# Optimization experiments

Hardware: AMD Instinct MI355X
Metric: run time of the kernel (lower is better)

Reference implementation:

```python
import jax, jax.numpy as jnp
import numpy as np

N_VERTICES = 24  # hardcoded via torch.eye(24) in the original
K = 3


def normalized_adj(adj):
    # scipy version: L = (A @ D^-1/2).T @ D^-1/2 = D^-1/2 @ A^T @ D^-1/2
    d = adj.sum(axis=1)
    d_inv_sqrt = jnp.where(d > 0, 1.0 / jnp.sqrt(d), 0.0)
    return (adj * d_inv_sqrt[None, :]).T * d_inv_sqrt[None, :]


def cheb_polynomials(L, k_order):
    Ts = [jnp.eye(N_VERTICES, dtype=L.dtype), L]
    for _ in range(2, k_order):
        Ts.append(2.0 * L @ Ts[-1] - Ts[-2])
    return jnp.stack(Ts[:k_order])  # (K, N, N)


def setup_inputs() -> dict:
    key = jax.random.key(0)
    k1, k2, k3 = jax.random.split(key, 3)
    x = jax.random.normal(k1, (64, 32, N_VERTICES, 512), dtype=jnp.float32)
    adj = jax.random.uniform(k2, (N_VERTICES, N_VERTICES), dtype=jnp.float32)
    Theta = jax.random.normal(k3, (K, 32, 32), dtype=jnp.float32)
    return {"x": x, "adj": adj, "Theta": Theta}


def reference(x, adj, Theta):
    # x: (b, c, n, t); adj: (n, n); Theta: (K, c, o)
    L = normalized_adj(adj)
    T = cheb_polynomials(L, K)  # (K, n, m)
    # original per-timestep, per-k: rhs[b,m,c] = sum_n x[b,n,c] T_k[n,m];
    # out[b,m,o] += rhs @ Theta_k. Fused over t and k, final permute -> (b,o,m,t).
    out = jnp.einsum('knm,bcnt,kco->bomt', T, x, Theta)
    return out
```

## Files before the change

### kernel.cpp

```cpp
#include <hip/hip_runtime.h>
#include <hip/hip_bf16.h>
#include <stdint.h>


#define NV 24
#define CIN 32
#define COUT 32
#define TDIM 512
#define BATCH 64
#define MDIM 768
#define KD 768
#define BK 32
#define NKT (KD / BK)
#define BM 128
#define BLOB (BM * BK)
#define BT 64
#define KUN (KD / 8)
#define FSTR 66

typedef __attribute__((ext_vector_type(8))) short short8v;
typedef __attribute__((ext_vector_type(4))) float float4v;

__device__ inline unsigned short f2bf(float f) {
    unsigned int u = __float_as_uint(f);
    unsigned int r = (u + 0x7fffu + ((u >> 16) & 1u)) >> 16;
    return (unsigned short)r;
}

__global__ __launch_bounds__(256) void prep_w(const float* __restrict__ adj,
                                              const float* __restrict__ Theta,
                                              unsigned short* __restrict__ Wp) {
    __shared__ float adjS[NV * NV];
    __shared__ float disS[NV];
    __shared__ float LS[NV * NV];
    __shared__ float T2S[NV * NV];
    int tid = threadIdx.x;
    for (int e = tid; e < NV * NV; e += 256) adjS[e] = adj[e];
    __syncthreads();
    if (tid < NV) {
        float d = 0.f;
        for (int j = 0; j < NV; ++j) d += adjS[tid * NV + j];
        disS[tid] = (d > 0.f) ? rsqrtf(d) : 0.f;
    }
    __syncthreads();
    for (int e = tid; e < NV * NV; e += 256) {
        int i = e / NV, j = e % NV;
        LS[e] = disS[i] * adjS[j * NV + i] * disS[j];
    }
    __syncthreads();
    for (int e = tid; e < NV * NV; e += 256) {
        int i = e / NV, j = e % NV;
        float s = 0.f;
        for (int p = 0; p < NV; ++p) s += LS[i * NV + p] * LS[p * NV + j];
        T2S[e] = 2.f * s - (i == j ? 1.f : 0.f);
    }
    __syncthreads();
    int r0 = blockIdx.x * (MDIM / 64);
    for (int e = tid; e < (MDIM / 64) * KD; e += 256) {
        int lr = e / KD, col = e % KD;
        int row = r0 + lr;
        int o = row / NV, m = row % NV;
        int c = col / NV, n = col % NV;
        float th0 = Theta[0 * CIN * COUT + c * COUT + o];
        float th1 = Theta[1 * CIN * COUT + c * COUT + o];
        float th2 = Theta[2 * CIN * COUT + c * COUT + o];
        float v = (n == m ? th0 : 0.f) + LS[n * NV + m] * th1 + T2S[n * NV + m] * th2;
        size_t idx = (((size_t)(row >> 7) * NKT + (col >> 5)) * BM + (row & 127)) * BK + (col & 31);
        Wp[idx] = f2bf(v);
    }
}

#define GSTEP(KT, AC, AN)                                                      \
    do {                                                                       \
        int kx = (((KT) * 4 + quad) ^ s7);                                     \
        short8v bb[4];                                                         \
        _Pragma("unroll")                                                      \
        for (int j = 0; j < 4; ++j) bb[j] = Bsv[tj[j] + kx];                   \
        if ((KT) + 1 < NKT) {                                                  \
            _Pragma("unroll")                                                  \
            for (int i = 0; i < 6; ++i) AN[i] = Apv[aoff[i] + ((KT) + 1) * 512]; \
        }                                                                      \
        _Pragma("unroll")                                                      \
        for (int i = 0; i < 6; ++i)                                            \
            _Pragma("unroll")                                                  \
            for (int j = 0; j < 4; ++j)                                        \
                acc[i][j] = __builtin_amdgcn_mfma_f32_16x16x32_bf16(           \
                    AC[i], bb[j], acc[i][j], 0, 0, 0);                         \
    } while (0)

__global__ __launch_bounds__(512, 2) void gemm_fullm(const unsigned short* __restrict__ Wp,
                                                     const float* __restrict__ x,
                                                     float* __restrict__ out) {
    __shared__ __attribute__((aligned(16))) unsigned short Bs[BT * KUN * 8];
    __shared__ float LSf[192 * FSTR];

    int id = blockIdx.x;
    int b = id >> 3;
    int tt = id & 7;
    int tid = threadIdx.x;
    int w = tid >> 6;
    int lane = tid & 63;
    int quad = lane >> 4;
    int l16 = lane & 15;
    int t = lane;
    int s7 = l16 & 7;

    const float* xg = x + (size_t)b * KD * TDIM + (size_t)tt * BT;
    short8v* Bsv = (short8v*)Bs;

    for (int kc = 0; kc < 4; ++kc) {
        float2 v[12];
#pragma unroll
        for (int p = 0; p < 12; ++p) {
            int idx = p * 512 + tid;
            int kloc = idx >> 5, c2 = idx & 31;
            v[p] = *(const float2*)(xg + (size_t)(kc * 192 + kloc) * TDIM + c2 * 2);
        }
#pragma unroll
        for (int p = 0; p < 12; ++p) {
            int idx = p * 512 + tid;
            int kloc = idx >> 5, c2 = idx & 31;
            *(float2*)(&LSf[kloc * FSTR + c2 * 2]) = v[p];
        }
        __syncthreads();
#pragma unroll
        for (int c = 0; c < 3; ++c) {
            union { short8v s; __hip_bfloat162 h[4]; } u;
#pragma unroll
            for (int p = 0; p < 4; ++p) {
                float f0 = LSf[(w * 24 + c * 8 + 2 * p) * FSTR + t];
                float f1 = LSf[(w * 24 + c * 8 + 2 * p + 1) * FSTR + t];
                u.h[p] = __float22bfloat162_rn({f0, f1});
            }
            int ku = kc * 24 + w * 3 + c;
            Bsv[t * KUN + (ku ^ (t & 7))] = u.s;
        }
        __syncthreads();
    }

    const short8v* Apv = (const short8v*)Wp;
    int aoff[6];
#pragma unroll
    for (int i = 0; i < 6; ++i) {
        int r = w * 96 + i * 16 + l16;
        aoff[i] = (r >> 7) * (NKT * 512) + (r & 127) * 4 + quad;
    }
    int tj[4];
#pragma unroll
    for (int j = 0; j < 4; ++j) tj[j] = (j * 16 + l16) * KUN;

    const float4v zero4 = {0.f, 0.f, 0.f, 0.f};
    float4v acc[6][4];
#pragma unroll
    for (int i = 0; i < 6; ++i)
#pragma unroll
        for (int j = 0; j < 4; ++j) acc[i][j] = zero4;

    short8v Aev[6], Aod[6];
#pragma unroll
    for (int i = 0; i < 6; ++i) Aev[i] = Apv[aoff[i]];

    for (int kt = 0; kt < NKT; kt += 2) {
        GSTEP(kt, Aev, Aod);
        GSTEP(kt + 1, Aod, Aev);
    }

    float* outB = out + (size_t)b * MDIM * TDIM + (size_t)tt * BT;
    int rb0 = w * 96;
#pragma unroll
    for (int i = 0; i < 6; ++i) {
#pragma unroll
        for (int j = 0; j < 4; ++j) {
            int row0 = rb0 + i * 16 + quad * 4;
            int col = j * 16 + l16;
#pragma unroll
            for (int r = 0; r < 4; ++r)
                __builtin_nontemporal_store(acc[i][j][r],
                                            &outB[(size_t)(row0 + r) * TDIM + col]);
        }
    }
}

extern "C" void kernel_launch(void* const* d_in, const int* in_sizes, int n_in,
                              void* d_out, int out_size, void* d_ws, size_t ws_size,
                              hipStream_t stream) {
    const float* x = (const float*)d_in[0];
    const float* adj = (const float*)d_in[1];
    const float* Theta = (const float*)d_in[2];
    float* out = (float*)d_out;

    unsigned short* Wp = (unsigned short*)d_ws;

    prep_w<<<64, 256, 0, stream>>>(adj, Theta, Wp);
    gemm_fullm<<<BATCH * (TDIM / BT), 512, 0, stream>>>(Wp, x, out);
}
```

Measured before the change: 234.8 us.

## Interleave x-chunk staging with MFMA k-steps and prefetch next chunk

Restructures the fused kernel so each 192-row chunk of x is converted to bf16 and its six GEMM k-steps run right away. The next chunk's global loads (now float4 instead of float2) are issued before the barrier so they overlap with the MFMA work. The aim is to hide the serialized load-then-compute prologue. It also changes the LDS pad stride to 68 for 16-byte alignment and replaces the nontemporal output stores with ordinary stores in a different loop order. Keeping the prefetch registers live alongside the accumulators raises register pressure.

```diff
diff --git a/kernel.cpp b/kernel.cpp
--- a/kernel.cpp
+++ b/kernel.cpp
@@ -16,7 +16,7 @@
 #define BLOB (BM * BK)
 #define BT 64
 #define KUN (KD / 8)
-#define FSTR 66
+#define FSTR 68
 
 typedef __attribute__((ext_vector_type(8))) short short8v;
 typedef __attribute__((ext_vector_type(4))) float float4v;
@@ -88,11 +88,19 @@
                     AC[i], bb[j], acc[i][j], 0, 0, 0);                         \
     } while (0)
 
+#define LOADC(KC)                                                              \
+    _Pragma("unroll")                                                          \
+    for (int p = 0; p < 6; ++p) {                                              \
+        int idx = p * 512 + tid;                                               \
+        int kloc = idx >> 4, c4 = idx & 15;                                    \
+        vx[p] = *(const float4*)(xg + (size_t)((KC) * 192 + kloc) * TDIM + c4 * 4); \
+    }
+
 __global__ __launch_bounds__(512, 2) void gemm_fullm(const unsigned short* __restrict__ Wp,
                                                      const float* __restrict__ x,
                                                      float* __restrict__ out) {
     __shared__ __attribute__((aligned(16))) unsigned short Bs[BT * KUN * 8];
-    __shared__ float LSf[192 * FSTR];
+    __shared__ __attribute__((aligned(16))) float LSf[192 * FSTR];
 
     int id = blockIdx.x;
     int b = id >> 3;
@@ -108,19 +116,36 @@
     const float* xg = x + (size_t)b * KD * TDIM + (size_t)tt * BT;
     short8v* Bsv = (short8v*)Bs;
 
+    const short8v* Apv = (const short8v*)Wp;
+    int aoff[6];
+#pragma unroll
+    for (int i = 0; i < 6; ++i) {
+        int r = w * 96 + i * 16 + l16;
+        aoff[i] = (r >> 7) * (NKT * 512) + (r & 127) * 4 + quad;
+    }
+    int tj[4];
+#pragma unroll
+    for (int j = 0; j < 4; ++j) tj[j] = (j * 16 + l16) * KUN;
+
+    const float4v zero4 = {0.f, 0.f, 0.f, 0.f};
+    float4v acc[6][4];
+#pragma unroll
+    for (int i = 0; i < 6; ++i)
+#pragma unroll
+        for (int j = 0; j < 4; ++j) acc[i][j] = zero4;
+
+    float4 vx[6];
+    LOADC(0);
+    short8v Aev[6], Aod[6];
+#pragma unroll
+    for (int i = 0; i < 6; ++i) Aev[i] = Apv[aoff[i]];
+
     for (int kc = 0; kc < 4; ++kc) {
-        float2 v[12];
-#pragma unroll
-        for (int p = 0; p < 12; ++p) {
+#pragma unroll
+        for (int p = 0; p < 6; ++p) {
             int idx = p * 512 + tid;
-            int kloc = idx >> 5, c2 = idx & 31;
-            v[p] = *(const float2*)(xg + (size_t)(kc * 192 + kloc) * TDIM + c2 * 2);
-        }
-#pragma unroll
-        for (int p = 0; p < 12; ++p) {
-            int idx = p * 512 + tid;
-            int kloc = idx >> 5, c2 = idx & 31;
-            *(float2*)(&LSf[kloc * FSTR + c2 * 2]) = v[p];
+            int kloc = idx >> 4, c4 = idx & 15;
+            *(float4*)(&LSf[kloc * FSTR + c4 * 4]) = vx[p];
         }
         __syncthreads();
 #pragma unroll
@@ -135,34 +160,16 @@
             int ku = kc * 24 + w * 3 + c;
             Bsv[t * KUN + (ku ^ (t & 7))] = u.s;
         }
+        if (kc + 1 < 4) { LOADC(kc + 1); }
         __syncthreads();
-    }
-
-    const short8v* Apv = (const short8v*)Wp;
-    int aoff[6];
-#pragma unroll
-    for (int i = 0; i < 6; ++i) {
-        int r = w * 96 + i * 16 + l16;
-        aoff[i] = (r >> 7) * (NKT * 512) + (r & 127) * 4 + quad;
-    }
-    int tj[4];
-#pragma unroll
-    for (int j = 0; j < 4; ++j) tj[j] = (j * 16 + l16) * KUN;
-
-    const float4v zero4 = {0.f, 0.f, 0.f, 0.f};
-    float4v acc[6][4];
-#pragma unroll
-    for (int i = 0; i < 6; ++i)
-#pragma unroll
-        for (int j = 0; j < 4; ++j) acc[i][j] = zero4;
-
-    short8v Aev[6], Aod[6];
-#pragma unroll
-    for (int i = 0; i < 6; ++i) Aev[i] = Apv[aoff[i]];
-
-    for (int kt = 0; kt < NKT; kt += 2) {
-        GSTEP(kt, Aev, Aod);
-        GSTEP(kt + 1, Aod, Aev);
+
+        int k0 = kc * 6;
+        GSTEP(k0 + 0, Aev, Aod);
+        GSTEP(k0 + 1, Aod, Aev);
+        GSTEP(k0 + 2, Aev, Aod);
+        GSTEP(k0 + 3, Aod, Aev);
+        GSTEP(k0 + 4, Aev, Aod);
+        GSTEP(k0 + 5, Aod, Aev);
     }
 
     float* outB = out + (size_t)b * MDIM * TDIM + (size_t)tt * BT;
@@ -170,13 +177,13 @@
 #pragma unroll
     for (int i = 0; i < 6; ++i) {
 #pragma unroll
-        for (int j = 0; j < 4; ++j) {
-            int row0 = rb0 + i * 16 + quad * 4;
-            int col = j * 16 + l16;
-#pragma unroll
-            for (int r = 0; r < 4; ++r)
-                __builtin_nontemporal_store(acc[i][j][r],
-                                            &outB[(size_t)(row0 + r) * TDIM + col]);
+        for (int r = 0; r < 4; ++r) {
+            int row = rb0 + i * 16 + quad * 4 + r;
+#pragma unroll
+            for (int j = 0; j < 4; ++j) {
+                int col = j * 16 + l16;
+                outB[(size_t)row * TDIM + col] = acc[i][j][r];
+            }
         }
     }
 }
```

Measured after the change: 245.0 us. +4.3%, slower.
